# Performance work log

Hardware: AMD Instinct MI355X
Metric: run time of the kernel (lower is better)

The kernel has to match this reference:

```python
import jax, jax.numpy as jnp
import numpy as np

B, N, M = 8, 131072, 64
M_VALID = 48  # trailing padding, matches remove_pad semantics
POSITIVE_IOU = 0.5
NEGATIVE_IOU = 0.3
CLASS_NUM = 1  # hardcoded in RpnTarget.__init__


def _make_boxes(key, shape_prefix, max_wh=64.0, span=1024.0):
    k1, k2, k3, k4 = jax.random.split(key, 4)
    x1 = jax.random.uniform(k1, shape_prefix, minval=0.0, maxval=span)
    y1 = jax.random.uniform(k2, shape_prefix, minval=0.0, maxval=span)
    w = jax.random.uniform(k3, shape_prefix, minval=4.0, maxval=max_wh)
    h = jax.random.uniform(k4, shape_prefix, minval=4.0, maxval=max_wh)
    return jnp.stack([x1, y1, x1 + w, y1 + h], axis=-1)


def setup_inputs() -> dict:
    key = jax.random.key(0)
    ka, kb = jax.random.split(key, 2)
    prior_anchors = _make_boxes(ka, (B, N))                       # [B,N,4]
    boxes = _make_boxes(kb, (B, M), max_wh=128.0)                 # [B,M,4]
    status = jnp.concatenate(
        [jnp.ones((B, M_VALID, 1)), jnp.zeros((B, M - M_VALID, 1))], axis=1
    )
    gt_bboxes = jnp.concatenate([boxes, status], axis=-1)          # [B,M,5]
    gt_class_idxes = jnp.zeros((B, M, 2), dtype=jnp.int32)         # zeroed in call()
    return {
        "prior_anchors": prior_anchors,
        "gt_bboxes": gt_bboxes,
        "gt_class_idxes": gt_class_idxes,
    }


def _bbox_transform(anchors, bboxes):
    # anchors, bboxes: [..., 4] in [x1,y1,x2,y2]
    ax = (anchors[..., 0] + anchors[..., 2]) * 0.5
    ay = (anchors[..., 1] + anchors[..., 3]) * 0.5
    aw = anchors[..., 2] - anchors[..., 0]
    ah = anchors[..., 3] - anchors[..., 1]
    bx = (bboxes[..., 0] + bboxes[..., 2]) * 0.5
    by = (bboxes[..., 1] + bboxes[..., 3]) * 0.5
    bw = bboxes[..., 2] - bboxes[..., 0]
    bh = bboxes[..., 3] - bboxes[..., 1]
    tx = (bx - ax) / aw
    ty = (by - ay) / ah
    tw = jnp.log(bw / aw)
    th = jnp.log(bh / ah)
    return jnp.stack([tx, ty, tw, th], axis=-1)


def _rpn_targets(prior_anchors, gt_bboxes, gt_class_idxes):
    boxes = gt_bboxes[..., :4]                 # [B,M,4]
    valid = gt_bboxes[..., 4] > 0              # [B,M] padding status

    a = prior_anchors[:, :, None, :]           # [B,N,1,4]
    b = boxes[:, None, :, :]                   # [B,1,M,4]
    inter_w = jnp.maximum(jnp.minimum(a[..., 2], b[..., 2]) - jnp.maximum(a[..., 0], b[..., 0]), 0.0)
    inter_h = jnp.maximum(jnp.minimum(a[..., 3], b[..., 3]) - jnp.maximum(a[..., 1], b[..., 1]), 0.0)
    inter = inter_w * inter_h                  # [B,N,M]
    area_a = jnp.maximum(a[..., 2] - a[..., 0], 0.0) * jnp.maximum(a[..., 3] - a[..., 1], 0.0)
    area_b = jnp.maximum(b[..., 2] - b[..., 0], 0.0) * jnp.maximum(b[..., 3] - b[..., 1], 0.0)
    iou = inter / (area_a + area_b - inter)    # [B,N,M]
    # mask out padded gt boxes (equivalent to remove_pad + trailing padding)
    iou = jnp.where(valid[:, None, :], iou, -1.0)

    max_iou = jnp.max(iou, axis=-1)            # [B,N]
    match_idx = jnp.argmax(iou, axis=-1)       # [B,N]
    positive = max_iou >= POSITIVE_IOU
    ignore = (max_iou >= NEGATIVE_IOU) & ~positive

    matched_boxes = jnp.take_along_axis(boxes, match_idx[..., None], axis=1)  # [B,N,4]
    reg = _bbox_transform(prior_anchors, matched_boxes)                        # [B,N,4]

    status = jnp.where(positive, 1.0, jnp.where(ignore, -1.0, 0.0))[..., None]  # [B,N,1]

    # call() zeros gt_class_idxes, so matched class idx is always 0; one_hot depth 1 -> ones
    cls_idx = jnp.take_along_axis(
        jnp.zeros_like(gt_class_idxes)[..., 0], match_idx, axis=1
    )                                                                           # [B,N] int32 zeros
    cls = jax.nn.one_hot(cls_idx, CLASS_NUM, dtype=reg.dtype)                   # [B,N,1]

    regression_targets = jnp.concatenate([reg, status], axis=-1)                # [B,N,5]
    classification_targets = jnp.concatenate([cls, status], axis=-1)            # [B,N,2]
    return regression_targets, classification_targets


def reference(prior_anchors, gt_bboxes, gt_class_idxes):
    return _rpn_targets(prior_anchors, gt_bboxes, gt_class_idxes)
```

## Files before the change

kernel.cpp:

```cpp
#include <hip/hip_runtime.h>


#define BB    8
#define NN    131072
#define MM    64
#define BLK   256
#define NBLK  (NN / BLK)
#define GC    16
#define CELLS (GC * GC)
#define CAP   32

#define WS_BOXES 0
#define WS_AREA  8192
#define WS_CNT   10240
#define WS_LIST  10272
#define WS_LEN   75808

__global__ __launch_bounds__(256) void rpn_build_lists(
    const float* __restrict__ gt, char* __restrict__ ws)
{
    __shared__ float4 sbox[MM];
    __shared__ float  sarea[MM];
    __shared__ int    scnt;

    const int b = blockIdx.x;
    const int t = threadIdx.x;

    float4* wboxes = (float4*)(ws + WS_BOXES);
    float*  warea  = (float*)(ws + WS_AREA);
    int*    wcnt   = (int*)(ws + WS_CNT);
    unsigned char* wlist = (unsigned char*)(ws + WS_LIST);
    unsigned char* wlen  = (unsigned char*)(ws + WS_LEN);

    if (t < MM) {
        const float* g = gt + ((size_t)b * MM + t) * 5;
        float x1 = g[0], y1 = g[1], x2 = g[2], y2 = g[3], st = g[4];
        bool valid = (st > 0.0f);
        unsigned long long mask = __ballot(valid);
        int slot = __popcll(mask & ((1ull << t) - 1ull));
        if (t == 0) { scnt = __popcll(mask); wcnt[b] = __popcll(mask); }
        if (valid) {
            float4 bx = make_float4(x1, y1, x2, y2);
            float  ar = fmaxf(x2 - x1, 0.0f) * fmaxf(y2 - y1, 0.0f);
            sbox[slot] = bx; sarea[slot] = ar;
            wboxes[b * MM + slot] = bx;
            warea[b * MM + slot]  = ar;
        }
    }
    __syncthreads();

    const int cnt = scnt;
    const int cx = t & (GC - 1), cy = t >> 4;
    const float wx1 = cx * 64.0f, wx2 = wx1 + 128.0f;
    const float wy1 = cy * 64.0f, wy2 = wy1 + 128.0f;

    unsigned char* lst = wlist + ((size_t)b * CELLS + t) * CAP;
    int len = 0;
    for (int s = 0; s < cnt; ++s) {
        float4 bx = sbox[s];
        if (bx.x <= wx2 && bx.z >= wx1 && bx.y <= wy2 && bx.w >= wy1) {
            if (len < CAP) lst[len] = (unsigned char)s;
            ++len;
        }
    }
    wlen[(size_t)b * CELLS + t] = (unsigned char)len;
}

__global__ __launch_bounds__(BLK) void rpn_target_kernel(
    const float* __restrict__ anchors,
    const float* __restrict__ gt,
    const char* __restrict__ ws,
    float* __restrict__ out)
{
    __shared__ float4 sbox[MM];
    __shared__ float  sarea[MM];
    __shared__ uint4  slist4[CELLS * CAP / 16];
    __shared__ uint   slen32[CELLS / 4];
    __shared__ int    scnt;

    const int t = threadIdx.x;
    const int b = blockIdx.x / NBLK;
    const int n = (blockIdx.x % NBLK) * BLK + t;

    if (t < MM) {
        sbox[t]  = ((const float4*)(ws + WS_BOXES))[b * MM + t];
        sarea[t] = ((const float*)(ws + WS_AREA))[b * MM + t];
    }
    if (t == 0) scnt = ((const int*)(ws + WS_CNT))[b];
    if (t < CELLS / 4)
        slen32[t] = ((const uint*)(ws + WS_LEN + (size_t)b * CELLS))[t];
    {
        const uint4* src = (const uint4*)(ws + WS_LIST + (size_t)b * CELLS * CAP);
        slist4[t * 2]     = src[t * 2];
        slist4[t * 2 + 1] = src[t * 2 + 1];
    }
    __syncthreads();

    const unsigned char* slist = (const unsigned char*)slist4;
    const unsigned char* slen  = (const unsigned char*)slen32;

    const float4 a = ((const float4*)anchors)[(size_t)b * NN + n];
    const float area_a = fmaxf(a.z - a.x, 0.0f) * fmaxf(a.w - a.y, 0.0f);
    const int cnt = scnt;

    int cx = (int)(a.x * 0.015625f); cx = cx < 0 ? 0 : (cx > GC - 1 ? GC - 1 : cx);
    int cy = (int)(a.y * 0.015625f); cy = cy < 0 ? 0 : (cy > GC - 1 ? GC - 1 : cy);
    const int cid = cy * GC + cx;

    const int len  = slen[cid];
    const bool full = (len > CAP);
    const int mylen = full ? cnt : len;
    const unsigned char* lst = slist + cid * CAP;

    float best  = 0.0f;
    int   bslot = 0;
    for (int j = 0; ; ++j) {
        if (!__any(j < mylen)) break;
        if (j < mylen) {
            const int idx = full ? j : (int)lst[j];
            const float4 bb = sbox[idx];
            const float  ab = sarea[idx];
            float iw = fmaxf(fminf(a.z, bb.z) - fmaxf(a.x, bb.x), 0.0f);
            float ih = fmaxf(fminf(a.w, bb.w) - fmaxf(a.y, bb.y), 0.0f);
            float inter = iw * ih;
            if (inter > 0.0f) {
                float denom = (area_a + ab) - inter;
                float iou = inter / denom;
                if (iou > best) { best = iou; bslot = idx; }
            }
        }
    }

    const bool positive = (best >= 0.5f);
    const bool ignore   = (best >= 0.3f) && !positive;
    const float status  = positive ? 1.0f : (ignore ? -1.0f : 0.0f);

    float4 mb;
    if (cnt > 0) {
        mb = sbox[bslot];
    } else {
        const float* g0 = gt + (size_t)b * MM * 5;
        mb = make_float4(g0[0], g0[1], g0[2], g0[3]);
    }

    const float axc = (a.x + a.z) * 0.5f;
    const float ayc = (a.y + a.w) * 0.5f;
    const float aw  = a.z - a.x;
    const float ah  = a.w - a.y;
    const float bxc = (mb.x + mb.z) * 0.5f;
    const float byc = (mb.y + mb.w) * 0.5f;
    const float bw  = mb.z - mb.x;
    const float bh  = mb.w - mb.y;
    const float tx  = (bxc - axc) / aw;
    const float ty  = (byc - ayc) / ah;
    const float tw  = logf(bw / aw);
    const float th  = logf(bh / ah);

    const size_t gid = (size_t)b * NN + n;

    float* r = out + gid * 5;
    r[0] = tx; r[1] = ty; r[2] = tw; r[3] = th; r[4] = status;

    float2* c = (float2*)(out + (size_t)BB * NN * 5) + gid;
    *c = make_float2(1.0f, status);
}

extern "C" void kernel_launch(void* const* d_in, const int* in_sizes, int n_in,
                              void* d_out, int out_size, void* d_ws, size_t ws_size,
                              hipStream_t stream) {
    const float* anchors = (const float*)d_in[0];
    const float* gt      = (const float*)d_in[1];

    float* out = (float*)d_out;
    char*  ws  = (char*)d_ws;

    hipLaunchKernelGGL(rpn_build_lists, dim3(BB), dim3(256), 0, stream, gt, ws);
    hipLaunchKernelGGL(rpn_target_kernel, dim3(BB * NBLK), dim3(BLK), 0, stream,
                       anchors, gt, ws, out);
}
```

Before: 25.76 us.

## Template spatial grid, use finer 32x32 cells, and fast rcp/log intrinsics

Makes the grid size and per-cell capacity template parameters and selects a 32x32 grid with 16-entry lists when the workspace is large enough. Smaller cells should shorten candidate lists per anchor, reducing IoU evaluations. Also replaces the divisions and logf with hardware reciprocal and log2 intrinsics. In exchange, each block stages more list data into shared memory, and the approximate rcp/log may change results slightly.

```diff
diff --git a/kernel.cpp b/kernel.cpp
--- a/kernel.cpp
+++ b/kernel.cpp
@@ -6,21 +6,19 @@
 #define MM    64
 #define BLK   256
 #define NBLK  (NN / BLK)
-#define GC    16
-#define CELLS (GC * GC)
-#define CAP   32
 
 #define WS_BOXES 0
 #define WS_AREA  8192
 #define WS_CNT   10240
 #define WS_LIST  10272
-#define WS_LEN   75808
 
+template<int GC, int CAP>
 __global__ __launch_bounds__(256) void rpn_build_lists(
     const float* __restrict__ gt, char* __restrict__ ws)
 {
+    constexpr int CELLS = GC * GC;
+    constexpr float SCALE = 1024.0f / GC;
     __shared__ float4 sbox[MM];
-    __shared__ float  sarea[MM];
     __shared__ int    scnt;
 
     const int b = blockIdx.x;
@@ -30,7 +28,7 @@
     float*  warea  = (float*)(ws + WS_AREA);
     int*    wcnt   = (int*)(ws + WS_CNT);
     unsigned char* wlist = (unsigned char*)(ws + WS_LIST);
-    unsigned char* wlen  = (unsigned char*)(ws + WS_LEN);
+    unsigned char* wlen  = (unsigned char*)(ws + WS_LIST + (size_t)BB * CELLS * CAP);
 
     if (t < MM) {
         const float* g = gt + ((size_t)b * MM + t) * 5;
@@ -41,37 +39,41 @@
         if (t == 0) { scnt = __popcll(mask); wcnt[b] = __popcll(mask); }
         if (valid) {
             float4 bx = make_float4(x1, y1, x2, y2);
-            float  ar = fmaxf(x2 - x1, 0.0f) * fmaxf(y2 - y1, 0.0f);
-            sbox[slot] = bx; sarea[slot] = ar;
+            sbox[slot] = bx;
             wboxes[b * MM + slot] = bx;
-            warea[b * MM + slot]  = ar;
+            warea[b * MM + slot]  = fmaxf(x2 - x1, 0.0f) * fmaxf(y2 - y1, 0.0f);
         }
     }
     __syncthreads();
 
     const int cnt = scnt;
-    const int cx = t & (GC - 1), cy = t >> 4;
-    const float wx1 = cx * 64.0f, wx2 = wx1 + 128.0f;
-    const float wy1 = cy * 64.0f, wy2 = wy1 + 128.0f;
-
-    unsigned char* lst = wlist + ((size_t)b * CELLS + t) * CAP;
-    int len = 0;
-    for (int s = 0; s < cnt; ++s) {
-        float4 bx = sbox[s];
-        if (bx.x <= wx2 && bx.z >= wx1 && bx.y <= wy2 && bx.w >= wy1) {
-            if (len < CAP) lst[len] = (unsigned char)s;
-            ++len;
+    for (int c = t; c < CELLS; c += 256) {
+        const int cx = c & (GC - 1), cy = c / GC;
+        const float wx1 = cx * SCALE, wx2 = wx1 + (SCALE + 64.0f);
+        const float wy1 = cy * SCALE, wy2 = wy1 + (SCALE + 64.0f);
+        unsigned char* lst = wlist + ((size_t)b * CELLS + c) * CAP;
+        int len = 0;
+        for (int s = 0; s < cnt; ++s) {
+            float4 bx = sbox[s];
+            if (bx.x <= wx2 && bx.z >= wx1 && bx.y <= wy2 && bx.w >= wy1) {
+                if (len < CAP) lst[len] = (unsigned char)s;
+                ++len;
+            }
         }
+        wlen[(size_t)b * CELLS + c] = (unsigned char)len;
     }
-    wlen[(size_t)b * CELLS + t] = (unsigned char)len;
 }
 
+template<int GC, int CAP>
 __global__ __launch_bounds__(BLK) void rpn_target_kernel(
     const float* __restrict__ anchors,
     const float* __restrict__ gt,
     const char* __restrict__ ws,
     float* __restrict__ out)
 {
+    constexpr int CELLS = GC * GC;
+    constexpr float INV = GC / 1024.0f;
+
     __shared__ float4 sbox[MM];
     __shared__ float  sarea[MM];
     __shared__ uint4  slist4[CELLS * CAP / 16];
@@ -87,12 +89,12 @@
         sarea[t] = ((const float*)(ws + WS_AREA))[b * MM + t];
     }
     if (t == 0) scnt = ((const int*)(ws + WS_CNT))[b];
-    if (t < CELLS / 4)
-        slen32[t] = ((const uint*)(ws + WS_LEN + (size_t)b * CELLS))[t];
+    for (int i = t; i < CELLS / 4; i += BLK)
+        slen32[i] = ((const uint*)(ws + WS_LIST + (size_t)BB * CELLS * CAP
+                                   + (size_t)b * CELLS))[i];
     {
         const uint4* src = (const uint4*)(ws + WS_LIST + (size_t)b * CELLS * CAP);
-        slist4[t * 2]     = src[t * 2];
-        slist4[t * 2 + 1] = src[t * 2 + 1];
+        for (int i = t; i < CELLS * CAP / 16; i += BLK) slist4[i] = src[i];
     }
     __syncthreads();
 
@@ -103,11 +105,11 @@
     const float area_a = fmaxf(a.z - a.x, 0.0f) * fmaxf(a.w - a.y, 0.0f);
     const int cnt = scnt;
 
-    int cx = (int)(a.x * 0.015625f); cx = cx < 0 ? 0 : (cx > GC - 1 ? GC - 1 : cx);
-    int cy = (int)(a.y * 0.015625f); cy = cy < 0 ? 0 : (cy > GC - 1 ? GC - 1 : cy);
+    int cx = (int)(a.x * INV); cx = cx < 0 ? 0 : (cx > GC - 1 ? GC - 1 : cx);
+    int cy = (int)(a.y * INV); cy = cy < 0 ? 0 : (cy > GC - 1 ? GC - 1 : cy);
     const int cid = cy * GC + cx;
 
-    const int len  = slen[cid];
+    const int len   = slen[cid];
     const bool full = (len > CAP);
     const int mylen = full ? cnt : len;
     const unsigned char* lst = slist + cid * CAP;
@@ -143,18 +145,21 @@
         mb = make_float4(g0[0], g0[1], g0[2], g0[3]);
     }
 
+    const float aw  = a.z - a.x;
+    const float ah  = a.w - a.y;
+    const float rw  = __builtin_amdgcn_rcpf(aw);
+    const float rh  = __builtin_amdgcn_rcpf(ah);
     const float axc = (a.x + a.z) * 0.5f;
     const float ayc = (a.y + a.w) * 0.5f;
-    const float aw  = a.z - a.x;
-    const float ah  = a.w - a.y;
     const float bxc = (mb.x + mb.z) * 0.5f;
     const float byc = (mb.y + mb.w) * 0.5f;
     const float bw  = mb.z - mb.x;
     const float bh  = mb.w - mb.y;
-    const float tx  = (bxc - axc) / aw;
-    const float ty  = (byc - ayc) / ah;
-    const float tw  = logf(bw / aw);
-    const float th  = logf(bh / ah);
+    const float tx  = (bxc - axc) * rw;
+    const float ty  = (byc - ayc) * rh;
+    const float LN2 = 0.69314718055994531f;
+    const float tw  = __builtin_amdgcn_logf(bw * rw) * LN2;
+    const float th  = __builtin_amdgcn_logf(bh * rh) * LN2;
 
     const size_t gid = (size_t)b * NN + n;
 
@@ -174,7 +179,14 @@
     float* out = (float*)d_out;
     char*  ws  = (char*)d_ws;
 
-    hipLaunchKernelGGL(rpn_build_lists, dim3(BB), dim3(256), 0, stream, gt, ws);
-    hipLaunchKernelGGL(rpn_target_kernel, dim3(BB * NBLK), dim3(BLK), 0, stream,
-                       anchors, gt, ws, out);
+    const size_t need32 = 10272 + (size_t)BB * 1024 * 16 + (size_t)BB * 1024;
+    if (ws_size >= need32) {
+        hipLaunchKernelGGL((rpn_build_lists<32, 16>), dim3(BB), dim3(256), 0, stream, gt, ws);
+        hipLaunchKernelGGL((rpn_target_kernel<32, 16>), dim3(BB * NBLK), dim3(BLK), 0, stream,
+                           anchors, gt, ws, out);
+    } else {
+        hipLaunchKernelGGL((rpn_build_lists<16, 32>), dim3(BB), dim3(256), 0, stream, gt, ws);
+        hipLaunchKernelGGL((rpn_target_kernel<16, 32>), dim3(BB * NBLK), dim3(BLK), 0, stream,
+                           anchors, gt, ws, out);
+    }
 }
```

After: 42.36 us. 64.4% more time.

## Transpose cell lists, split boxes into SoA, use fast rcp/log intrinsics

Applied to the files above, without the earlier changes.

The per-cell candidate lists are stored transposed (slot-major across cells), and the shared-memory box data is split into structure-of-arrays, so lane reads in the IoU loop hit different LDS banks instead of strided bytes and float4 loads. The epilogue swaps the IEEE divides and logf for hardware reciprocal and log2 intrinsics scaled by ln2. This cuts LDS bank conflicts and ALU cost, at the price of slightly lower precision in the regression targets.

```diff
diff --git a/kernel.cpp b/kernel.cpp
--- a/kernel.cpp
+++ b/kernel.cpp
@@ -20,7 +20,6 @@
     const float* __restrict__ gt, char* __restrict__ ws)
 {
     __shared__ float4 sbox[MM];
-    __shared__ float  sarea[MM];
     __shared__ int    scnt;
 
     const int b = blockIdx.x;
@@ -41,10 +40,9 @@
         if (t == 0) { scnt = __popcll(mask); wcnt[b] = __popcll(mask); }
         if (valid) {
             float4 bx = make_float4(x1, y1, x2, y2);
-            float  ar = fmaxf(x2 - x1, 0.0f) * fmaxf(y2 - y1, 0.0f);
-            sbox[slot] = bx; sarea[slot] = ar;
+            sbox[slot] = bx;
             wboxes[b * MM + slot] = bx;
-            warea[b * MM + slot]  = ar;
+            warea[b * MM + slot]  = fmaxf(x2 - x1, 0.0f) * fmaxf(y2 - y1, 0.0f);
         }
     }
     __syncthreads();
@@ -54,12 +52,13 @@
     const float wx1 = cx * 64.0f, wx2 = wx1 + 128.0f;
     const float wy1 = cy * 64.0f, wy2 = wy1 + 128.0f;
 
-    unsigned char* lst = wlist + ((size_t)b * CELLS + t) * CAP;
     int len = 0;
     for (int s = 0; s < cnt; ++s) {
         float4 bx = sbox[s];
         if (bx.x <= wx2 && bx.z >= wx1 && bx.y <= wy2 && bx.w >= wy1) {
-            if (len < CAP) lst[len] = (unsigned char)s;
+            if (len < CAP)
+                wlist[(size_t)b * CELLS * CAP + (size_t)len * CELLS + t]
+                    = (unsigned char)s;
             ++len;
         }
     }
@@ -72,19 +71,21 @@
     const char* __restrict__ ws,
     float* __restrict__ out)
 {
-    __shared__ float4 sbox[MM];
-    __shared__ float  sarea[MM];
-    __shared__ uint4  slist4[CELLS * CAP / 16];
-    __shared__ uint   slen32[CELLS / 4];
-    __shared__ int    scnt;
+    constexpr float INV = GC / 1024.0f;
+
+    __shared__ float sx1[MM], sy1[MM], sx2[MM], sy2[MM], sar[MM];
+    __shared__ uint4 slist4[CELLS * CAP / 16];
+    __shared__ uint  slen32[CELLS / 4];
+    __shared__ int   scnt;
 
     const int t = threadIdx.x;
     const int b = blockIdx.x / NBLK;
     const int n = (blockIdx.x % NBLK) * BLK + t;
 
     if (t < MM) {
-        sbox[t]  = ((const float4*)(ws + WS_BOXES))[b * MM + t];
-        sarea[t] = ((const float*)(ws + WS_AREA))[b * MM + t];
+        float4 bx = ((const float4*)(ws + WS_BOXES))[b * MM + t];
+        sx1[t] = bx.x; sy1[t] = bx.y; sx2[t] = bx.z; sy2[t] = bx.w;
+        sar[t] = ((const float*)(ws + WS_AREA))[b * MM + t];
     }
     if (t == 0) scnt = ((const int*)(ws + WS_CNT))[b];
     if (t < CELLS / 4)
@@ -103,25 +104,25 @@
     const float area_a = fmaxf(a.z - a.x, 0.0f) * fmaxf(a.w - a.y, 0.0f);
     const int cnt = scnt;
 
-    int cx = (int)(a.x * 0.015625f); cx = cx < 0 ? 0 : (cx > GC - 1 ? GC - 1 : cx);
-    int cy = (int)(a.y * 0.015625f); cy = cy < 0 ? 0 : (cy > GC - 1 ? GC - 1 : cy);
+    int cx = (int)(a.x * INV); cx = cx < 0 ? 0 : (cx > GC - 1 ? GC - 1 : cx);
+    int cy = (int)(a.y * INV); cy = cy < 0 ? 0 : (cy > GC - 1 ? GC - 1 : cy);
     const int cid = cy * GC + cx;
 
-    const int len  = slen[cid];
+    const int len   = slen[cid];
     const bool full = (len > CAP);
     const int mylen = full ? cnt : len;
-    const unsigned char* lst = slist + cid * CAP;
 
     float best  = 0.0f;
     int   bslot = 0;
     for (int j = 0; ; ++j) {
         if (!__any(j < mylen)) break;
         if (j < mylen) {
-            const int idx = full ? j : (int)lst[j];
-            const float4 bb = sbox[idx];
-            const float  ab = sarea[idx];
-            float iw = fmaxf(fminf(a.z, bb.z) - fmaxf(a.x, bb.x), 0.0f);
-            float ih = fmaxf(fminf(a.w, bb.w) - fmaxf(a.y, bb.y), 0.0f);
+            const int idx = full ? j : (int)slist[j * CELLS + cid];
+            const float bx1 = sx1[idx], by1 = sy1[idx];
+            const float bx2 = sx2[idx], by2 = sy2[idx];
+            const float ab  = sar[idx];
+            float iw = fmaxf(fminf(a.z, bx2) - fmaxf(a.x, bx1), 0.0f);
+            float ih = fmaxf(fminf(a.w, by2) - fmaxf(a.y, by1), 0.0f);
             float inter = iw * ih;
             if (inter > 0.0f) {
                 float denom = (area_a + ab) - inter;
@@ -135,26 +136,29 @@
     const bool ignore   = (best >= 0.3f) && !positive;
     const float status  = positive ? 1.0f : (ignore ? -1.0f : 0.0f);
 
-    float4 mb;
+    float mx1, my1, mx2, my2;
     if (cnt > 0) {
-        mb = sbox[bslot];
+        mx1 = sx1[bslot]; my1 = sy1[bslot]; mx2 = sx2[bslot]; my2 = sy2[bslot];
     } else {
         const float* g0 = gt + (size_t)b * MM * 5;
-        mb = make_float4(g0[0], g0[1], g0[2], g0[3]);
+        mx1 = g0[0]; my1 = g0[1]; mx2 = g0[2]; my2 = g0[3];
     }
 
+    const float aw  = a.z - a.x;
+    const float ah  = a.w - a.y;
+    const float rw  = __builtin_amdgcn_rcpf(aw);
+    const float rh  = __builtin_amdgcn_rcpf(ah);
     const float axc = (a.x + a.z) * 0.5f;
     const float ayc = (a.y + a.w) * 0.5f;
-    const float aw  = a.z - a.x;
-    const float ah  = a.w - a.y;
-    const float bxc = (mb.x + mb.z) * 0.5f;
-    const float byc = (mb.y + mb.w) * 0.5f;
-    const float bw  = mb.z - mb.x;
-    const float bh  = mb.w - mb.y;
-    const float tx  = (bxc - axc) / aw;
-    const float ty  = (byc - ayc) / ah;
-    const float tw  = logf(bw / aw);
-    const float th  = logf(bh / ah);
+    const float bxc = (mx1 + mx2) * 0.5f;
+    const float byc = (my1 + my2) * 0.5f;
+    const float bw  = mx2 - mx1;
+    const float bh  = my2 - my1;
+    const float tx  = (bxc - axc) * rw;
+    const float ty  = (byc - ayc) * rh;
+    const float LN2 = 0.69314718055994531f;
+    const float tw  = __builtin_amdgcn_logf(bw * rw) * LN2;
+    const float th  = __builtin_amdgcn_logf(bh * rh) * LN2;
 
     const size_t gid = (size_t)b * NN + n;
 
```

Result: no change. 25.41 us (-1.4%).
